# Kernel optimization log

Hardware: AMD Instinct MI355X
Metric: run time of the kernel (lower is better)

Reference implementation:

```python
import jax, jax.numpy as jnp
import numpy as np

N_NODES = 100000


def gcn_conv(x, edge_index, W, b):
    """PyG-style GCNConv: symmetric-normalized A+I propagation of x @ W, plus bias."""
    n = x.shape[0]
    src, dst = edge_index[0], edge_index[1]
    loops = jnp.arange(n, dtype=src.dtype)
    src = jnp.concatenate([src, loops])  # add self loops
    dst = jnp.concatenate([dst, loops])
    deg = jax.ops.segment_sum(jnp.ones_like(src, dtype=x.dtype), dst, num_segments=n)
    dinv = jnp.where(deg > 0, jax.lax.rsqrt(deg), 0.0)
    norm = dinv[src] * dinv[dst]  # [E+n]
    h = x @ W  # [n, out]
    msg = h[src] * norm[:, None]  # gather + scale
    out = jax.ops.segment_sum(msg, dst, num_segments=n)  # scatter-add
    return out + b


def setup_inputs() -> dict:
    key = jax.random.key(0)
    ks = jax.random.split(key, 5)
    x = jax.random.normal(ks[0], (N_NODES, 4), dtype=jnp.float32)
    edge_index = jax.random.randint(ks[1], (2, 3200000), 0, N_NODES, dtype=jnp.int64)
    W1 = jax.random.normal(ks[2], (4, 64), dtype=jnp.float32) * 0.5
    b1 = jnp.zeros((64,), dtype=jnp.float32)
    W2 = jax.random.normal(ks[3], (64, 32), dtype=jnp.float32) * 0.125
    b2 = jnp.zeros((32,), dtype=jnp.float32)
    return {"x": x, "edge_index": edge_index, "W1": W1, "b1": b1, "W2": W2, "b2": b2}


def reference(x, edge_index, W1, b1, W2, b2):
    h = gcn_conv(x, edge_index, W1, b1)
    h = jax.nn.relu(h)
    # F.dropout with training=False is identity (eval-mode reference)
    h = gcn_conv(h, edge_index, W2, b2)
    return jnp.mean(h, axis=0)  # [32]
```

## Files before the change

### kernel.cpp

```cpp
#include <hip/hip_runtime.h>

#define ST 1024
#define EPB 8192
#define HT 1024
#define FT 1024
#define S_LOG 8
#define S 256
#define CAP 8912
#define MAXB 512
#define FXS 8388608.0f
#define FXI 1.1920929e-7f

__device__ __forceinline__ void gAtomAdd(float* p, float v) {
    unsafeAtomicAdd(p, v);
}

__global__ void __launch_bounds__(ST) k_sctr2(
        const int4* __restrict__ src4, const int4* __restrict__ dst4, int E,
        int* __restrict__ cur_d, int* __restrict__ cur_s,
        unsigned* __restrict__ rec_d, unsigned* __restrict__ rec_s, int nb) {
    __shared__ unsigned lrec[EPB];
    __shared__ unsigned short lbkt[EPB];
    __shared__ int cnt[MAXB];
    __shared__ int lst[MAXB];
    __shared__ int gb[MAXB];
    __shared__ int wsum[8];
    int t = threadIdx.x;
    int lane = t & 63, wv = t >> 6;
    int E4 = E >> 2;
    int b4 = blockIdx.x * (EPB / 4);
    int m = min(EPB, E - blockIdx.x * EPB);

    int4 dk[2], sk[2];
    bool v[2];
    #pragma unroll
    for (int k = 0; k < 2; ++k) {
        int idx = b4 + k * ST + t;
        v[k] = idx < E4;
        if (v[k]) { dk[k] = dst4[idx]; sk[k] = src4[idx]; }
    }

    for (int ph = 0; ph < 2; ++ph) {
        int* cursor = ph ? cur_s : cur_d;
        unsigned* rec = ph ? rec_s : rec_d;
        if (t < MAXB) cnt[t] = 0;
        __syncthreads();
        int rk[8];
        #pragma unroll
        for (int k = 0; k < 2; ++k) {
            if (v[k]) {
                int4 K = ph ? sk[k] : dk[k];
                rk[4 * k + 0] = atomicAdd(&cnt[K.x >> S_LOG], 1);
                rk[4 * k + 1] = atomicAdd(&cnt[K.y >> S_LOG], 1);
                rk[4 * k + 2] = atomicAdd(&cnt[K.z >> S_LOG], 1);
                rk[4 * k + 3] = atomicAdd(&cnt[K.w >> S_LOG], 1);
            }
        }
        __syncthreads();
        int c = 0, ic = 0;
        if (t < MAXB) {
            c = cnt[t]; ic = c;
            #pragma unroll
            for (int o = 1; o < 64; o <<= 1) {
                int u = __shfl_up(ic, o);
                if (lane >= o) ic += u;
            }
            if (lane == 63) wsum[wv] = ic;
        }
        __syncthreads();
        if (t < MAXB) {
            int pre = 0;
            #pragma unroll
            for (int k = 0; k < 7; ++k) pre += (k < wv) ? wsum[k] : 0;
            ic += pre;
            lst[t] = ic - c;
            gb[t] = (c > 0) ? t * CAP + atomicAdd(&cursor[t], c) : 0;
        }
        __syncthreads();
        #pragma unroll
        for (int k = 0; k < 2; ++k) {
            if (v[k]) {
                int4 K = ph ? sk[k] : dk[k];
                int4 P = ph ? dk[k] : sk[k];
                int bb, p;
                bb = K.x >> S_LOG; p = lst[bb] + rk[4 * k + 0];
                lrec[p] = ((unsigned)P.x << S_LOG) | (unsigned)(K.x & (S - 1));
                lbkt[p] = (unsigned short)bb;
                bb = K.y >> S_LOG; p = lst[bb] + rk[4 * k + 1];
                lrec[p] = ((unsigned)P.y << S_LOG) | (unsigned)(K.y & (S - 1));
                lbkt[p] = (unsigned short)bb;
                bb = K.z >> S_LOG; p = lst[bb] + rk[4 * k + 2];
                lrec[p] = ((unsigned)P.z << S_LOG) | (unsigned)(K.z & (S - 1));
                lbkt[p] = (unsigned short)bb;
                bb = K.w >> S_LOG; p = lst[bb] + rk[4 * k + 3];
                lrec[p] = ((unsigned)P.w << S_LOG) | (unsigned)(K.w & (S - 1));
                lbkt[p] = (unsigned short)bb;
            }
        }
        __syncthreads();
        for (int i = t; i < m; i += ST) {
            int bb = lbkt[i];
            rec[gb[bb] + (i - lst[bb])] = lrec[i];
        }
        __syncthreads();
    }
}

__global__ void __launch_bounds__(HT) k_hist(
        const unsigned* __restrict__ rec_d, const int* __restrict__ cur_d,
        const float4* __restrict__ x, float* __restrict__ dinv,
        float4* __restrict__ y, int n) {
    __shared__ int cnt[S];
    int b = blockIdx.x, t = threadIdx.x;
    if (t < S) cnt[t] = 0;
    __syncthreads();
    int lo = b * CAP;
    int m = cur_d[b];
    int m4 = m >> 2;
    const uint4* rec4 = (const uint4*)(rec_d + lo);
    for (int i = t; i < m4; i += HT) {
        uint4 r = rec4[i];
        atomicAdd(&cnt[r.x & (S - 1)], 1);
        atomicAdd(&cnt[r.y & (S - 1)], 1);
        atomicAdd(&cnt[r.z & (S - 1)], 1);
        atomicAdd(&cnt[r.w & (S - 1)], 1);
    }
    for (int i = (m4 << 2) + t; i < m; i += HT)
        atomicAdd(&cnt[rec_d[lo + i] & (S - 1)], 1);
    __syncthreads();
    int nd = (b << S_LOG) + t;
    if (t < S && nd < n) {
        float dv = rsqrtf((float)cnt[t] + 1.0f);
        dinv[nd] = dv;
        float4 xi = x[nd];
        y[nd] = make_float4(dv * xi.x, dv * xi.y, dv * xi.z, dv * xi.w);
    }
}

__global__ void __launch_bounds__(FT) k_fuse(
        const unsigned* __restrict__ rec_d, const unsigned* __restrict__ rec_s,
        const int* __restrict__ cur_d, const int* __restrict__ cur_s,
        const float4* __restrict__ y, const float* __restrict__ dinv,
        const float* __restrict__ W1, const float* __restrict__ b1,
        const float* __restrict__ W2, const float* __restrict__ b2,
        float* __restrict__ g, int* __restrict__ done,
        float* __restrict__ out, float inv_n, int n) {
    __shared__ unsigned lrec[CAP];
    __shared__ int cnt[S];
    __shared__ int nst[S];
    __shared__ int ia[S];
    __shared__ float4 lp1[S];
    __shared__ float red[FT];
    __shared__ int wsum[4];
    __shared__ int sticket;
    int b = blockIdx.x, t = threadIdx.x;
    int lane = t & 63, wv = t >> 6;
    if (t < S) { cnt[t] = 0; ia[t] = 0; }
    __syncthreads();
    int lo = b * CAP;
    int md = cur_d[b];
    unsigned rv[9]; int rr[9];
    #pragma unroll
    for (int k = 0; k < 9; ++k) {
        int i = t + k * FT;
        if (i < md) {
            unsigned r = rec_d[lo + i];
            rv[k] = r;
            rr[k] = atomicAdd(&cnt[r & (S - 1)], 1);
        }
    }
    __syncthreads();
    int c = 0, ic = 0;
    if (t < S) {
        c = cnt[t]; ic = c;
        #pragma unroll
        for (int o = 1; o < 64; o <<= 1) {
            int u = __shfl_up(ic, o);
            if (lane >= o) ic += u;
        }
        if (lane == 63) wsum[wv] = ic;
    }
    __syncthreads();
    if (t < S) {
        int pre = 0;
        #pragma unroll
        for (int k = 0; k < 3; ++k) pre += (k < wv) ? wsum[k] : 0;
        ic += pre;
        cnt[t] = ic;
        nst[t] = ic - c;
    }
    __syncthreads();
    #pragma unroll
    for (int k = 0; k < 9; ++k) {
        int i = t + k * FT;
        if (i < md) lrec[nst[rv[k] & (S - 1)] + rr[k]] = rv[k] >> S_LOG;
    }
    int ms = cur_s[b];
    int ms4 = ms >> 2;
    const uint4* rs4 = (const uint4*)(rec_s + lo);
    for (int i = t; i < ms4; i += FT) {
        uint4 r = rs4[i];
        int d0 = (int)(dinv[r.x >> S_LOG] * FXS + 0.5f);
        int d1 = (int)(dinv[r.y >> S_LOG] * FXS + 0.5f);
        int d2 = (int)(dinv[r.z >> S_LOG] * FXS + 0.5f);
        int d3 = (int)(dinv[r.w >> S_LOG] * FXS + 0.5f);
        atomicAdd(&ia[r.x & (S - 1)], d0);
        atomicAdd(&ia[r.y & (S - 1)], d1);
        atomicAdd(&ia[r.z & (S - 1)], d2);
        atomicAdd(&ia[r.w & (S - 1)], d3);
    }
    for (int i = (ms4 << 2) + t; i < ms; i += FT) {
        unsigned r = rec_s[lo + i];
        atomicAdd(&ia[r & (S - 1)], (int)(dinv[r >> S_LOG] * FXS + 0.5f));
    }
    __syncthreads();
    int node = t >> 2, q = t & 3;
    int nd = (b << S_LOG) + node;
    if (nd < n) {
        int j1 = cnt[node];
        int j = nst[node] + q;
        float a0 = 0.0f, a1 = 0.0f, a2 = 0.0f, a3 = 0.0f;
        for (; j + 12 < j1; j += 16) {
            int s0 = lrec[j], s1 = lrec[j + 4], s2 = lrec[j + 8], s3 = lrec[j + 12];
            float4 y0 = y[s0], y1 = y[s1], y2 = y[s2], y3 = y[s3];
            a0 += y0.x + y1.x + y2.x + y3.x;
            a1 += y0.y + y1.y + y2.y + y3.y;
            a2 += y0.z + y1.z + y2.z + y3.z;
            a3 += y0.w + y1.w + y2.w + y3.w;
        }
        for (; j < j1; j += 4) {
            float4 ys = y[lrec[j]];
            a0 += ys.x; a1 += ys.y; a2 += ys.z; a3 += ys.w;
        }
        a0 += __shfl_down(a0, 2); a1 += __shfl_down(a1, 2);
        a2 += __shfl_down(a2, 2); a3 += __shfl_down(a3, 2);
        a0 += __shfl_down(a0, 1); a1 += __shfl_down(a1, 1);
        a2 += __shfl_down(a2, 1); a3 += __shfl_down(a3, 1);
        if (q == 0) {
            float di = dinv[nd];
            lp1[node] = make_float4(di * a0, di * a1, di * a2, di * a3);
        }
    }
    __syncthreads();
    int cch = t & 63, w = t >> 6;
    float w0 = W1[cch], w1 = W1[64 + cch], w2 = W1[128 + cch], w3 = W1[192 + cch];
    float bb = b1[cch];
    int nb0 = b << S_LOG;
    float facc = 0.0f;
    for (int k = w; k < S; k += 16) {
        int ndk = nb0 + k;
        if (ndk >= n) break;
        float di = dinv[ndk];
        float4 p = lp1[k];
        float4 yi = y[ndk];
        float h0 = fmaf(di, yi.x, p.x);
        float h1 = fmaf(di, yi.y, p.y);
        float h2 = fmaf(di, yi.z, p.z);
        float h3 = fmaf(di, yi.w, p.w);
        float h = fmaf(h0, w0, fmaf(h1, w1, fmaf(h2, w2, fmaf(h3, w3, bb))));
        h = fmaxf(h, 0.0f);
        float ak = (float)ia[k] * FXI;
        float wi = fmaf(di, ak, di * di);
        facc = fmaf(wi, h, facc);
    }
    red[t] = facc;
    __syncthreads();
    if (t < 64) {
        float s = red[t];
        #pragma unroll
        for (int o = 1; o < 16; ++o) s += red[t + 64 * o];
        gAtomAdd(&g[t], s);
    }
    __syncthreads();
    if (t == 0) {
        __threadfence();
        sticket = atomicAdd(done, 1);
    }
    __syncthreads();
    if (sticket == (int)gridDim.x - 1) {
        if (t < 32) {
            float acc = 0.0f;
            #pragma unroll
            for (int cc = 0; cc < 64; ++cc) {
                float gv = __hip_atomic_load(&g[cc], __ATOMIC_RELAXED,
                                             __HIP_MEMORY_SCOPE_AGENT);
                acc = fmaf(gv, W2[cc * 32 + t], acc);
            }
            out[t] = fmaf(acc, inv_n, b2[t]);
        }
    }
}

extern "C" void kernel_launch(void* const* d_in, const int* in_sizes, int n_in,
                              void* d_out, int out_size, void* d_ws, size_t ws_size,
                              hipStream_t stream) {
    const float* x  = (const float*)d_in[0];
    const int*   ei = (const int*)d_in[1];
    const float* W1 = (const float*)d_in[2];
    const float* b1 = (const float*)d_in[3];
    const float* W2 = (const float*)d_in[4];
    const float* b2 = (const float*)d_in[5];
    float* out = (float*)d_out;

    int n = in_sizes[0] / 4;
    int E = in_sizes[1] / 2;
    const int* src = ei;
    const int* dst = ei + E;
    int NB = (n + S - 1) >> S_LOG;

    char* ws = (char*)d_ws;
    int* cur_d = (int*)ws;
    int* cur_s = cur_d + 512;
    float* g   = (float*)(cur_s + 512);
    int* done  = (int*)(g + 64);
    size_t ctrl = 1600;
    unsigned* rec_d = (unsigned*)ws + ctrl;
    unsigned* rec_s = rec_d + (size_t)NB * CAP;
    float* y    = (float*)(rec_s + (size_t)NB * CAP);
    float* dinv = y + 4 * (size_t)n;

    int NSB = (E + EPB - 1) / EPB;

    hipMemsetAsync(ws, 0, ctrl * 4, stream);
    k_sctr2<<<NSB, ST, 0, stream>>>((const int4*)src, (const int4*)dst, E,
                                    cur_d, cur_s, rec_d, rec_s, NB);
    k_hist<<<NB, HT, 0, stream>>>(rec_d, cur_d, (const float4*)x, dinv,
                                  (float4*)y, n);
    k_fuse<<<NB, FT, 0, stream>>>(rec_d, rec_s, cur_d, cur_s,
                                  (const float4*)y, dinv, W1, b1, W2, b2,
                                  g, done, out, 1.0f / (float)n, n);
}
```

Measured before the change: 150.2 us.

## Fuse degree histogram into main kernel via grid-wide atomic barrier

Removes the separate k_hist kernel. k_fuse already counts in-degrees per node bucket, so it now computes dinv and y itself, publishes them, then spins on a global atomic counter until every block has arrived. It also drops the last-block ticket reduction in favour of a tiny k_final launch. This saves one full pass over rec_d and a kernel boundary, but adds a software grid barrier that deadlocks unless all ~391 blocks of 1024 threads are resident at once.

```diff
diff --git a/kernel.cpp b/kernel.cpp
--- a/kernel.cpp
+++ b/kernel.cpp
@@ -2,7 +2,6 @@
 
 #define ST 1024
 #define EPB 8192
-#define HT 1024
 #define FT 1024
 #define S_LOG 8
 #define S 256
@@ -106,53 +105,21 @@
     }
 }
 
-__global__ void __launch_bounds__(HT) k_hist(
-        const unsigned* __restrict__ rec_d, const int* __restrict__ cur_d,
-        const float4* __restrict__ x, float* __restrict__ dinv,
-        float4* __restrict__ y, int n) {
-    __shared__ int cnt[S];
-    int b = blockIdx.x, t = threadIdx.x;
-    if (t < S) cnt[t] = 0;
-    __syncthreads();
-    int lo = b * CAP;
-    int m = cur_d[b];
-    int m4 = m >> 2;
-    const uint4* rec4 = (const uint4*)(rec_d + lo);
-    for (int i = t; i < m4; i += HT) {
-        uint4 r = rec4[i];
-        atomicAdd(&cnt[r.x & (S - 1)], 1);
-        atomicAdd(&cnt[r.y & (S - 1)], 1);
-        atomicAdd(&cnt[r.z & (S - 1)], 1);
-        atomicAdd(&cnt[r.w & (S - 1)], 1);
-    }
-    for (int i = (m4 << 2) + t; i < m; i += HT)
-        atomicAdd(&cnt[rec_d[lo + i] & (S - 1)], 1);
-    __syncthreads();
-    int nd = (b << S_LOG) + t;
-    if (t < S && nd < n) {
-        float dv = rsqrtf((float)cnt[t] + 1.0f);
-        dinv[nd] = dv;
-        float4 xi = x[nd];
-        y[nd] = make_float4(dv * xi.x, dv * xi.y, dv * xi.z, dv * xi.w);
-    }
-}
-
 __global__ void __launch_bounds__(FT) k_fuse(
         const unsigned* __restrict__ rec_d, const unsigned* __restrict__ rec_s,
         const int* __restrict__ cur_d, const int* __restrict__ cur_s,
-        const float4* __restrict__ y, const float* __restrict__ dinv,
+        const float4* __restrict__ x, float* __restrict__ dinv,
+        float4* __restrict__ y,
         const float* __restrict__ W1, const float* __restrict__ b1,
-        const float* __restrict__ W2, const float* __restrict__ b2,
-        float* __restrict__ g, int* __restrict__ done,
-        float* __restrict__ out, float inv_n, int n) {
+        float* __restrict__ g, int* __restrict__ bar, int n) {
     __shared__ unsigned lrec[CAP];
     __shared__ int cnt[S];
     __shared__ int nst[S];
     __shared__ int ia[S];
+    __shared__ float s_dinv[S];
     __shared__ float4 lp1[S];
     __shared__ float red[FT];
     __shared__ int wsum[4];
-    __shared__ int sticket;
     int b = blockIdx.x, t = threadIdx.x;
     int lane = t & 63, wv = t >> 6;
     if (t < S) { cnt[t] = 0; ia[t] = 0; }
@@ -188,13 +155,32 @@
         ic += pre;
         cnt[t] = ic;
         nst[t] = ic - c;
-    }
-    __syncthreads();
+        float dv = rsqrtf((float)c + 1.0f);
+        s_dinv[t] = dv;
+        int nd = (b << S_LOG) + t;
+        if (nd < n) {
+            dinv[nd] = dv;
+            float4 xi = x[nd];
+            y[nd] = make_float4(dv * xi.x, dv * xi.y, dv * xi.z, dv * xi.w);
+        }
+    }
+    __syncthreads();
+    if (t == 0) {
+        __threadfence();
+        __hip_atomic_fetch_add(bar, 1, __ATOMIC_RELEASE, __HIP_MEMORY_SCOPE_AGENT);
+    }
     #pragma unroll
     for (int k = 0; k < 9; ++k) {
         int i = t + k * FT;
         if (i < md) lrec[nst[rv[k] & (S - 1)] + rr[k]] = rv[k] >> S_LOG;
     }
+    __syncthreads();
+    if (t == 0) {
+        while (__hip_atomic_load(bar, __ATOMIC_ACQUIRE,
+                                 __HIP_MEMORY_SCOPE_AGENT) < (int)gridDim.x) {}
+        __threadfence();
+    }
+    __syncthreads();
     int ms = cur_s[b];
     int ms4 = ms >> 2;
     const uint4* rs4 = (const uint4*)(rec_s + lo);
@@ -237,7 +223,7 @@
         a0 += __shfl_down(a0, 1); a1 += __shfl_down(a1, 1);
         a2 += __shfl_down(a2, 1); a3 += __shfl_down(a3, 1);
         if (q == 0) {
-            float di = dinv[nd];
+            float di = s_dinv[node];
             lp1[node] = make_float4(di * a0, di * a1, di * a2, di * a3);
         }
     }
@@ -250,7 +236,7 @@
     for (int k = w; k < S; k += 16) {
         int ndk = nb0 + k;
         if (ndk >= n) break;
-        float di = dinv[ndk];
+        float di = s_dinv[k];
         float4 p = lp1[k];
         float4 yi = y[ndk];
         float h0 = fmaf(di, yi.x, p.x);
@@ -271,23 +257,16 @@
         for (int o = 1; o < 16; ++o) s += red[t + 64 * o];
         gAtomAdd(&g[t], s);
     }
-    __syncthreads();
-    if (t == 0) {
-        __threadfence();
-        sticket = atomicAdd(done, 1);
-    }
-    __syncthreads();
-    if (sticket == (int)gridDim.x - 1) {
-        if (t < 32) {
-            float acc = 0.0f;
-            #pragma unroll
-            for (int cc = 0; cc < 64; ++cc) {
-                float gv = __hip_atomic_load(&g[cc], __ATOMIC_RELAXED,
-                                             __HIP_MEMORY_SCOPE_AGENT);
-                acc = fmaf(gv, W2[cc * 32 + t], acc);
-            }
-            out[t] = fmaf(acc, inv_n, b2[t]);
-        }
+}
+
+__global__ void k_final(const float* __restrict__ g, const float* __restrict__ W2,
+                        const float* __restrict__ b2, float* __restrict__ out, float inv_n) {
+    int j = threadIdx.x;
+    if (j < 32) {
+        float a = 0.0f;
+        #pragma unroll
+        for (int c = 0; c < 64; ++c) a = fmaf(g[c], W2[c * 32 + j], a);
+        out[j] = fmaf(a, inv_n, b2[j]);
     }
 }
 
@@ -312,7 +291,7 @@
     int* cur_d = (int*)ws;
     int* cur_s = cur_d + 512;
     float* g   = (float*)(cur_s + 512);
-    int* done  = (int*)(g + 64);
+    int* bar   = (int*)(g + 64);
     size_t ctrl = 1600;
     unsigned* rec_d = (unsigned*)ws + ctrl;
     unsigned* rec_s = rec_d + (size_t)NB * CAP;
@@ -324,9 +303,8 @@
     hipMemsetAsync(ws, 0, ctrl * 4, stream);
     k_sctr2<<<NSB, ST, 0, stream>>>((const int4*)src, (const int4*)dst, E,
                                     cur_d, cur_s, rec_d, rec_s, NB);
-    k_hist<<<NB, HT, 0, stream>>>(rec_d, cur_d, (const float4*)x, dinv,
-                                  (float4*)y, n);
     k_fuse<<<NB, FT, 0, stream>>>(rec_d, rec_s, cur_d, cur_s,
-                                  (const float4*)y, dinv, W1, b1, W2, b2,
-                                  g, done, out, 1.0f / (float)n, n);
-}
+                                  (const float4*)x, dinv, (float4*)y,
+                                  W1, b1, g, bar, n);
+    k_final<<<1, 64, 0, stream>>>(g, W2, b2, out, 1.0f / (float)n);
+}
```

New measurement: 199.0 us. +32.5%, slower.
